# Performance work log

Hardware: AMD Instinct MI355X
Metric: run time of the kernel (lower is better)

The kernel has to match this reference:

```python
import jax, jax.numpy as jnp
import numpy as np
import math

B, T, D, H, K = 4, 2048, 1024, 16, 64

def setup_inputs() -> dict:
    key = jax.random.key(0)
    ks = jax.random.split(key, 6)
    scale = 1.0 / math.sqrt(D)  # keep logits in a sane range (torch code uses raw randn params)
    X = jax.random.normal(ks[0], (B, T, D), dtype=jnp.float32)
    Wq = jax.random.normal(ks[1], (H, D, K), dtype=jnp.float32) * scale
    Wk = jax.random.normal(ks[2], (H, D, K), dtype=jnp.float32) * scale
    Wv = jax.random.normal(ks[3], (H, D, K), dtype=jnp.float32) * scale
    Wo = jax.random.normal(ks[4], (H * K, H * K), dtype=jnp.float32) * (1.0 / math.sqrt(H * K))
    bo = jnp.zeros((H * K,), dtype=jnp.float32)
    return {"X": X, "Wq": Wq, "Wk": Wk, "Wv": Wv, "Wo": Wo, "bo": bo}

def reference(X, Wq, Wk, Wv, Wo, bo):
    # per-head projections: [B,H,T,K]
    q = jnp.einsum('btc,nck->bntk', X, Wq)
    k = jnp.einsum('btc,nck->bntk', X, Wk)
    v = jnp.einsum('btc,nck->bntk', X, Wv)
    # full score matrix [B,H,T,T] with causal mask (query t attends to s <= t)
    scores = jnp.einsum('bntk,bnsk->bnts', q, k) / math.sqrt(K)
    causal = jnp.tril(jnp.ones((T, T), dtype=bool))
    scores = jnp.where(causal[None, None], scores, jnp.finfo(scores.dtype).min)
    attn = jax.nn.softmax(scores, axis=-1)
    out = jnp.einsum('bnts,bnsk->bntk', attn, v)  # [B,H,T,K]
    # concat heads along feature dim (head-major ordering, matches torch.cat over heads)
    out = jnp.transpose(out, (0, 2, 1, 3)).reshape(B, T, H * K)
    # output projection (torch nn.Linear: x @ W.T + b)
    return out @ Wo.T + bo
```

## Files before the change

### kernel.cpp

```cpp
#include <hip/hip_runtime.h>
#include <hip/hip_bf16.h>
#include <math.h>

#define B_SZ 4
#define T_SZ 2048
#define D_SZ 1024
#define H_SZ 16
#define K_SZ 64

typedef __attribute__((ext_vector_type(8))) short bf8_t;
typedef __attribute__((ext_vector_type(4))) float f4_t;

__device__ __forceinline__ ushort f2bf(float f) {
    union { float f; unsigned u; } v; v.f = f;
    return (ushort)((v.u + 0x7fffu + ((v.u >> 16) & 1u)) >> 16);
}

__device__ __forceinline__ uint cvt_pk_bf16(float lo, float hi) {
    uint r;
    asm("v_cvt_pk_bf16_f32 %0, %1, %2" : "=v"(r) : "v"(lo), "v"(hi));
    return r;
}

__device__ __forceinline__ void gld_lds16(const ushort* g, ushort* l) {
    __builtin_amdgcn_global_load_lds(
        (const __attribute__((address_space(1))) void*)g,
        (__attribute__((address_space(3))) void*)l, 16, 0, 0);
}

#define Q_PRESCALE 0.18033688011112042f

__global__ __launch_bounds__(256) void convert_bf16_kernel(
    const float* __restrict__ src, ushort* __restrict__ dst)
{
    const size_t i = ((size_t)blockIdx.x * 256 + threadIdx.x) * 8;
    float4 a = *(const float4*)(src + i);
    float4 b = *(const float4*)(src + i + 4);
    ushort o[8] = {f2bf(a.x), f2bf(a.y), f2bf(a.z), f2bf(a.w),
                   f2bf(b.x), f2bf(b.y), f2bf(b.z), f2bf(b.w)};
    *(uint4*)(dst + i) = *(const uint4*)o;
}

__global__ __launch_bounds__(256) void transpose_w_kernel(
    const float* __restrict__ Wq, const float* __restrict__ Wk,
    const float* __restrict__ Wv, ushort* __restrict__ WT)
{
    __shared__ __align__(16) float tile[64][68];
    const int tid = threadIdx.x;
    const int d0  = blockIdx.x * 64;
    const int g   = blockIdx.y;
    const int sel = g >> 4, h = g & 15;
    const float* W = (sel == 0 ? Wq : (sel == 1 ? Wk : Wv)) + (size_t)h * D_SZ * K_SZ;

    {
        const int r = tid >> 2, ks = (tid & 3) * 16;
        const float4* src = (const float4*)(W + (size_t)(d0 + r) * 64 + ks);
        float4* dst = (float4*)&tile[r][ks];
        dst[0] = src[0]; dst[1] = src[1]; dst[2] = src[2]; dst[3] = src[3];
    }
    __syncthreads();
    {
        const int k = tid >> 2, ds = (tid & 3) * 16;
        ushort o[16];
        #pragma unroll
        for (int i = 0; i < 16; ++i) o[i] = f2bf(tile[ds + i][k]);
        uint4* dst = (uint4*)&WT[(size_t)(sel * 1024 + h * 64 + k) * 1024 + d0 + ds];
        dst[0] = ((const uint4*)o)[0];
        dst[1] = ((const uint4*)o)[1];
    }
}

__device__ __forceinline__ void gemm_bt_tile(
    const ushort* __restrict__ A, const ushort* __restrict__ Bt,
    int Kdim, int m0, int n0, ushort* As, ushort* Bs, f4_t acc[4][4])
{
    const int tid  = threadIdx.x;
    const int lane = tid & 63, wv = tid >> 6;
    const int l16  = lane & 15, quad = lane >> 4;
    const int wm   = (wv >> 1) * 64, wn = (wv & 1) * 64;
    const int sw   = (l16 >> 1) & 3;

    const int ra0 = tid >> 2,         qa0 = (tid & 3) ^ ((ra0 >> 1) & 3);
    const int ra1 = (tid + 256) >> 2, qa1 = (tid & 3) ^ ((ra1 >> 1) & 3);
    ushort* ldsA0 = As + (size_t)(wv * 64) * 8;
    ushort* ldsA1 = As + (size_t)(wv * 64 + 256) * 8;
    ushort* ldsB0 = Bs + (size_t)(wv * 64) * 8;
    ushort* ldsB1 = Bs + (size_t)(wv * 64 + 256) * 8;
    const ushort* gA0 = A  + (size_t)(m0 + ra0) * Kdim + qa0 * 8;
    const ushort* gA1 = A  + (size_t)(m0 + ra1) * Kdim + qa1 * 8;
    const ushort* gB0 = Bt + (size_t)(n0 + ra0) * Kdim + qa0 * 8;
    const ushort* gB1 = Bt + (size_t)(n0 + ra1) * Kdim + qa1 * 8;

    for (int k0 = 0; k0 < Kdim; k0 += 32) {
        __syncthreads();
        gld_lds16(gA0 + k0, ldsA0);
        gld_lds16(gA1 + k0, ldsA1);
        gld_lds16(gB0 + k0, ldsB0);
        gld_lds16(gB1 + k0, ldsB1);
        __syncthreads();

        bf8_t a[4], b[4];
        #pragma unroll
        for (int mt = 0; mt < 4; ++mt)
            a[mt] = *(const bf8_t*)&As[(wm + mt * 16 + l16) * 32 + ((quad ^ sw) * 8)];
        #pragma unroll
        for (int nt = 0; nt < 4; ++nt)
            b[nt] = *(const bf8_t*)&Bs[(wn + nt * 16 + l16) * 32 + ((quad ^ sw) * 8)];
        #pragma unroll
        for (int mt = 0; mt < 4; ++mt)
            #pragma unroll
            for (int nt = 0; nt < 4; ++nt)
                acc[mt][nt] = __builtin_amdgcn_mfma_f32_16x16x32_bf16(
                    a[mt], b[nt], acc[mt][nt], 0, 0, 0);
    }
}

__global__ __launch_bounds__(256) void gemm_qkv_kernel(
    const ushort* __restrict__ Xb, const ushort* __restrict__ WT,
    ushort* __restrict__ Qo, ushort* __restrict__ Ko, ushort* __restrict__ Vo)
{
    __shared__ __align__(16) ushort As[128 * 32];
    __shared__ __align__(16) ushort Bs[128 * 32];
    const int n0 = blockIdx.x * 128, m0 = blockIdx.y * 128;

    f4_t acc[4][4];
    #pragma unroll
    for (int i = 0; i < 4; ++i)
        #pragma unroll
        for (int j = 0; j < 4; ++j) acc[i][j] = (f4_t){0.f, 0.f, 0.f, 0.f};

    gemm_bt_tile(Xb, WT, 1024, m0, n0, As, Bs, acc);

    const int tid = threadIdx.x;
    const int lane = tid & 63, wv = tid >> 6;
    const int l16 = lane & 15, quad = lane >> 4;
    const int wm = (wv >> 1) * 64, wn = (wv & 1) * 64;
    const int sel = n0 >> 10;
    ushort* Out = (sel == 0 ? Qo : (sel == 1 ? Ko : Vo));
    const float osc = (sel == 0) ? Q_PRESCALE : 1.0f;

    #pragma unroll
    for (int nt = 0; nt < 4; ++nt) {
        const int col = n0 + wn + nt * 16 + l16;
        const int h = (col >> 6) & 15, kk = col & 63;
        #pragma unroll
        for (int mt = 0; mt < 4; ++mt) {
            #pragma unroll
            for (int r = 0; r < 4; ++r) {
                const int row = m0 + wm + mt * 16 + quad * 4 + r;
                const int bb = row >> 11, t = row & 2047;
                Out[((size_t)(bb * 16 + h) * 2048 + t) * 64 + kk] =
                    f2bf(acc[mt][nt][r] * osc);
            }
        }
    }
}

__global__ __launch_bounds__(256) void gemm_out_kernel(
    const ushort* __restrict__ Yb, const ushort* __restrict__ WoB,
    const float* __restrict__ bo, float* __restrict__ Out)
{
    __shared__ __align__(16) ushort As[128 * 32];
    __shared__ __align__(16) ushort Bs[128 * 32];
    const int n0 = blockIdx.x * 128, m0 = blockIdx.y * 128;

    f4_t acc[4][4];
    #pragma unroll
    for (int i = 0; i < 4; ++i)
        #pragma unroll
        for (int j = 0; j < 4; ++j) acc[i][j] = (f4_t){0.f, 0.f, 0.f, 0.f};

    gemm_bt_tile(Yb, WoB, 1024, m0, n0, As, Bs, acc);

    const int tid = threadIdx.x;
    const int lane = tid & 63, wv = tid >> 6;
    const int l16 = lane & 15, quad = lane >> 4;
    const int wm = (wv >> 1) * 64, wn = (wv & 1) * 64;

    #pragma unroll
    for (int nt = 0; nt < 4; ++nt) {
        const int col = n0 + wn + nt * 16 + l16;
        const float bias = bo[col];
        #pragma unroll
        for (int mt = 0; mt < 4; ++mt) {
            #pragma unroll
            for (int r = 0; r < 4; ++r) {
                const int row = m0 + wm + mt * 16 + quad * 4 + r;
                Out[(size_t)row * 1024 + col] = acc[mt][nt][r] + bias;
            }
        }
    }
}

__global__ __launch_bounds__(256) void transpose_v_kernel(
    const ushort* __restrict__ V, ushort* __restrict__ Vt)
{
    __shared__ __align__(16) ushort tile[64 * 74];
    const int tid = threadIdx.x;
    const int t0  = blockIdx.x * 64;
    const int bh  = blockIdx.y;

    {
        const int t = tid >> 2, ks = (tid & 3) * 16;
        const ushort* src = V + ((size_t)bh * T_SZ + t0 + t) * K_SZ + ks;
        uint4 a = *(const uint4*)src;
        uint4 b = *(const uint4*)(src + 8);
        uint* dst = (uint*)&tile[t * 74 + ks];
        dst[0] = a.x; dst[1] = a.y; dst[2] = a.z; dst[3] = a.w;
        dst[4] = b.x; dst[5] = b.y; dst[6] = b.z; dst[7] = b.w;
    }
    __syncthreads();
    {
        const int l = tid & 63, w = tid >> 6;
        #pragma unroll
        for (int kk = 0; kk < 16; ++kk) {
            const int k = w * 16 + kk;
            Vt[((size_t)bh * K_SZ + k) * T_SZ + t0 + l] = tile[l * 74 + k];
        }
    }
}

__global__ __launch_bounds__(64) void attn_mfma_kernel(
    const ushort* __restrict__ Qg, const ushort* __restrict__ Kg,
    const ushort* __restrict__ Vtg, ushort* __restrict__ Y)
{
    __shared__ __align__(16) ushort Ph[32 * 72];

    const int lane = threadIdx.x;
    const int l16  = lane & 15;
    const int quad = lane >> 4;

    const int lin  = blockIdx.x;
    const int xcd  = lin & 7;
    const int slot = (lin >> 3) & 31;
    const int u    = lin >> 8;
    const int bh   = xcd * 8 + (u & 7);
    const int j    = (u < 8) ? slot : 63 - slot;
    const int bb   = bh >> 4, h = bh & 15;

    const int trow = j * 32;

    const ushort* Kbh = Kg  + (size_t)bh * T_SZ * K_SZ;
    const ushort* Vbh = Vtg + (size_t)bh * K_SZ * T_SZ;

    bf8_t qa[2][2];
    #pragma unroll
    for (int mt = 0; mt < 2; ++mt) {
        const ushort* qp = Qg + ((size_t)bh * T_SZ + trow + mt * 16 + l16) * K_SZ + quad * 8;
        qa[mt][0] = *(const bf8_t*)qp;
        qa[mt][1] = *(const bf8_t*)(qp + 32);
    }

    f4_t O[2][4];
    float lp[2] = {0.f, 0.f};
    #pragma unroll
    for (int mt = 0; mt < 2; ++mt)
        #pragma unroll
        for (int dt = 0; dt < 4; ++dt) O[mt][dt] = (f4_t){0.f, 0.f, 0.f, 0.f};

    const int n_it = (trow + 32 + 63) >> 6;

    bf8_t kb[4][2], vb[4][2];
    #pragma unroll
    for (int nt = 0; nt < 4; ++nt)
        #pragma unroll
        for (int hh = 0; hh < 2; ++hh) {
            kb[nt][hh] = *(const bf8_t*)&Kbh[(size_t)(nt * 16 + l16) * K_SZ + hh * 32 + quad * 8];
            vb[nt][hh] = *(const bf8_t*)&Vbh[(size_t)(nt * 16 + l16) * T_SZ + hh * 32 + quad * 8];
        }

    for (int it = 0; it < n_it; ++it) {
        const int s0 = it * 64;
        const bool more = (it + 1 < n_it);
        const int  sn   = s0 + 64;

        f4_t S[4][2];
        #pragma unroll
        for (int nt = 0; nt < 4; ++nt)
            #pragma unroll
            for (int mt = 0; mt < 2; ++mt) {
                S[nt][mt] = (f4_t){0.f, 0.f, 0.f, 0.f};
                S[nt][mt] = __builtin_amdgcn_mfma_f32_16x16x32_bf16(
                    kb[nt][0], qa[mt][0], S[nt][mt], 0, 0, 0);
                S[nt][mt] = __builtin_amdgcn_mfma_f32_16x16x32_bf16(
                    kb[nt][1], qa[mt][1], S[nt][mt], 0, 0, 0);
            }

        if (more) {
            #pragma unroll
            for (int nt = 0; nt < 4; ++nt)
                #pragma unroll
                for (int hh = 0; hh < 2; ++hh)
                    kb[nt][hh] = *(const bf8_t*)&Kbh[
                        (size_t)(sn + nt * 16 + l16) * K_SZ + hh * 32 + quad * 8];
        }

        const bool diag = (s0 + 64 > trow);
        #pragma unroll
        for (int mt = 0; mt < 2; ++mt) {
            const int qg = trow + mt * 16 + l16;
            #pragma unroll
            for (int nt = 0; nt < 4; ++nt) {
                float p[4];
                if (diag) {
                    #pragma unroll
                    for (int r = 0; r < 4; ++r) {
                        float x = S[nt][mt][r];
                        if (s0 + nt * 16 + quad * 4 + r > qg) x = -1e30f;
                        p[r] = __builtin_amdgcn_exp2f(x);
                    }
                } else {
                    #pragma unroll
                    for (int r = 0; r < 4; ++r)
                        p[r] = __builtin_amdgcn_exp2f(S[nt][mt][r]);
                }
                lp[mt] += (p[0] + p[1]) + (p[2] + p[3]);
                uint2 pk;
                pk.x = cvt_pk_bf16(p[0], p[1]);
                pk.y = cvt_pk_bf16(p[2], p[3]);
                *(uint2*)&Ph[(mt * 16 + l16) * 72 + nt * 16 + quad * 4] = pk;
            }
        }
        asm volatile("" ::: "memory");
        bf8_t pa[2][2];
        #pragma unroll
        for (int mt = 0; mt < 2; ++mt) {
            const ushort* pr = &Ph[(mt * 16 + l16) * 72];
            pa[mt][0] = *(const bf8_t*)(pr + quad * 8);
            pa[mt][1] = *(const bf8_t*)(pr + 32 + quad * 8);
        }
        asm volatile("" ::: "memory");

        #pragma unroll
        for (int dt = 0; dt < 4; ++dt)
            #pragma unroll
            for (int mt = 0; mt < 2; ++mt) {
                O[mt][dt] = __builtin_amdgcn_mfma_f32_16x16x32_bf16(
                    pa[mt][0], vb[dt][0], O[mt][dt], 0, 0, 0);
                O[mt][dt] = __builtin_amdgcn_mfma_f32_16x16x32_bf16(
                    pa[mt][1], vb[dt][1], O[mt][dt], 0, 0, 0);
            }

        if (more) {
            #pragma unroll
            for (int nt = 0; nt < 4; ++nt)
                #pragma unroll
                for (int hh = 0; hh < 2; ++hh)
                    vb[nt][hh] = *(const bf8_t*)&Vbh[
                        (size_t)(nt * 16 + l16) * T_SZ + sn + hh * 32 + quad * 8];
        }
    }

    #pragma unroll
    for (int mt = 0; mt < 2; ++mt) {
        float s = lp[mt];
        s += __shfl_xor(s, 16);
        s += __shfl_xor(s, 32);
        const float inv = 1.f / s;
        float invr[4];
        #pragma unroll
        for (int r = 0; r < 4; ++r)
            invr[r] = __shfl(inv, quad * 4 + r);
        #pragma unroll
        for (int dt = 0; dt < 4; ++dt) {
            const int col = h * 64 + dt * 16 + l16;
            #pragma unroll
            for (int r = 0; r < 4; ++r) {
                const int tg = trow + mt * 16 + quad * 4 + r;
                Y[((size_t)(bb * T_SZ + tg)) * (H_SZ * K_SZ) + col] =
                    f2bf(O[mt][dt][r] * invr[r]);
            }
        }
    }
}

extern "C" void kernel_launch(void* const* d_in, const int* in_sizes, int n_in,
                              void* d_out, int out_size, void* d_ws, size_t ws_size,
                              hipStream_t stream) {
    const float* X  = (const float*)d_in[0];
    const float* Wq = (const float*)d_in[1];
    const float* Wk = (const float*)d_in[2];
    const float* Wv = (const float*)d_in[3];
    const float* Wo = (const float*)d_in[4];
    const float* bo = (const float*)d_in[5];
    float* out = (float*)d_out;

    const size_t NE = (size_t)B_SZ * H_SZ * T_SZ * K_SZ;
    ushort* Qb   = (ushort*)d_ws;
    ushort* Kb   = Qb + NE;
    ushort* Vb   = Kb + NE;
    ushort* Vtb  = Vb + NE;
    ushort* Yb   = Vtb + NE;
    ushort* Xb   = Yb + NE;
    ushort* WT   = Xb + NE;
    ushort* WoB  = WT + (size_t)3072 * 1024;

    convert_bf16_kernel<<<dim3(4096), 256, 0, stream>>>(X, Xb);
    convert_bf16_kernel<<<dim3(512), 256, 0, stream>>>(Wo, WoB);
    transpose_w_kernel<<<dim3(16, 48), 256, 0, stream>>>(Wq, Wk, Wv, WT);
    gemm_qkv_kernel<<<dim3(24, 64), 256, 0, stream>>>(Xb, WT, Qb, Kb, Vb);
    transpose_v_kernel<<<dim3(32, 64), 256, 0, stream>>>(Vb, Vtb);
    attn_mfma_kernel<<<dim3(4096), 64, 0, stream>>>(Qb, Kb, Vtb, Yb);
    gemm_out_kernel<<<dim3(8, 64), 256, 0, stream>>>(Yb, WoB, bo, out);
}
```

Baseline: 342.6 us.

## Balance causal attention work by pairing low and high query tiles per wave

Each wave now handles one 16-row query tile near the start and its mirrored tile near the end, so every wave runs a similar number of causal iterations. Each wave loads a K/V tile once and applies it to both query tiles, skipping the low tile once it is past its diagonal. Blocks hold two waves, and the grid changes from an XCD-swizzled 1D layout to a 2D (tile pair, batch-head) layout. This removes load imbalance between short and long causal rows, at the cost of the XCD-aware L2 locality mapping and possibly more K/V loads per query row.

```diff
diff --git a/kernel.cpp b/kernel.cpp
--- a/kernel.cpp
+++ b/kernel.cpp
@@ -220,45 +220,46 @@
     }
 }
 
-__global__ __launch_bounds__(64) void attn_mfma_kernel(
+__global__ __launch_bounds__(128) void attn_mfma_kernel(
     const ushort* __restrict__ Qg, const ushort* __restrict__ Kg,
     const ushort* __restrict__ Vtg, ushort* __restrict__ Y)
 {
-    __shared__ __align__(16) ushort Ph[32 * 72];
-
-    const int lane = threadIdx.x;
+    __shared__ __align__(16) ushort Ph[2][16 * 72];
+
+    const int tid  = threadIdx.x;
+    const int w    = tid >> 6;
+    const int lane = tid & 63;
     const int l16  = lane & 15;
     const int quad = lane >> 4;
 
-    const int lin  = blockIdx.x;
-    const int xcd  = lin & 7;
-    const int slot = (lin >> 3) & 31;
-    const int u    = lin >> 8;
-    const int bh   = xcd * 8 + (u & 7);
-    const int j    = (u < 8) ? slot : 63 - slot;
+    const int p    = (blockIdx.x << 1) | w;
+    const int bh   = blockIdx.y;
     const int bb   = bh >> 4, h = bh & 15;
 
-    const int trow = j * 32;
+    const int trowL = p * 16;
+    const int trowH = (127 - p) * 16;
 
     const ushort* Kbh = Kg  + (size_t)bh * T_SZ * K_SZ;
     const ushort* Vbh = Vtg + (size_t)bh * K_SZ * T_SZ;
 
-    bf8_t qa[2][2];
-    #pragma unroll
-    for (int mt = 0; mt < 2; ++mt) {
-        const ushort* qp = Qg + ((size_t)bh * T_SZ + trow + mt * 16 + l16) * K_SZ + quad * 8;
-        qa[mt][0] = *(const bf8_t*)qp;
-        qa[mt][1] = *(const bf8_t*)(qp + 32);
-    }
-
-    f4_t O[2][4];
-    float lp[2] = {0.f, 0.f};
-    #pragma unroll
-    for (int mt = 0; mt < 2; ++mt)
-        #pragma unroll
-        for (int dt = 0; dt < 4; ++dt) O[mt][dt] = (f4_t){0.f, 0.f, 0.f, 0.f};
-
-    const int n_it = (trow + 32 + 63) >> 6;
+    bf8_t qaL[2], qaH[2];
+    {
+        const ushort* qpL = Qg + ((size_t)bh * T_SZ + trowL + l16) * K_SZ + quad * 8;
+        const ushort* qpH = Qg + ((size_t)bh * T_SZ + trowH + l16) * K_SZ + quad * 8;
+        qaL[0] = *(const bf8_t*)qpL;  qaL[1] = *(const bf8_t*)(qpL + 32);
+        qaH[0] = *(const bf8_t*)qpH;  qaH[1] = *(const bf8_t*)(qpH + 32);
+    }
+
+    f4_t OL[4], OH[4];
+    float lpL = 0.f, lpH = 0.f;
+    #pragma unroll
+    for (int dt = 0; dt < 4; ++dt) {
+        OL[dt] = (f4_t){0.f, 0.f, 0.f, 0.f};
+        OH[dt] = (f4_t){0.f, 0.f, 0.f, 0.f};
+    }
+
+    ushort* myP = Ph[w];
+    const int n_it = (trowH + 16 + 63) >> 6;
 
     bf8_t kb[4][2], vb[4][2];
     #pragma unroll
@@ -269,22 +270,62 @@
             vb[nt][hh] = *(const bf8_t*)&Vbh[(size_t)(nt * 16 + l16) * T_SZ + hh * 32 + quad * 8];
         }
 
+    int s0 = 0;
+    auto qk = [&](const bf8_t (&qa)[2], f4_t (&S)[4]) {
+        #pragma unroll
+        for (int nt = 0; nt < 4; ++nt) {
+            S[nt] = (f4_t){0.f, 0.f, 0.f, 0.f};
+            S[nt] = __builtin_amdgcn_mfma_f32_16x16x32_bf16(kb[nt][0], qa[0], S[nt], 0, 0, 0);
+            S[nt] = __builtin_amdgcn_mfma_f32_16x16x32_bf16(kb[nt][1], qa[1], S[nt], 0, 0, 0);
+        }
+    };
+    auto sm_pv = [&](f4_t (&S)[4], f4_t (&O)[4], float& lp, int trow) {
+        const bool diag = (s0 + 64 > trow);
+        const int qg = trow + l16;
+        #pragma unroll
+        for (int nt = 0; nt < 4; ++nt) {
+            float pr[4];
+            if (diag) {
+                #pragma unroll
+                for (int r = 0; r < 4; ++r) {
+                    float x = S[nt][r];
+                    if (s0 + nt * 16 + quad * 4 + r > qg) x = -1e30f;
+                    pr[r] = __builtin_amdgcn_exp2f(x);
+                }
+            } else {
+                #pragma unroll
+                for (int r = 0; r < 4; ++r)
+                    pr[r] = __builtin_amdgcn_exp2f(S[nt][r]);
+            }
+            lp += (pr[0] + pr[1]) + (pr[2] + pr[3]);
+            uint2 pk;
+            pk.x = cvt_pk_bf16(pr[0], pr[1]);
+            pk.y = cvt_pk_bf16(pr[2], pr[3]);
+            *(uint2*)&myP[l16 * 72 + nt * 16 + quad * 4] = pk;
+        }
+        asm volatile("" ::: "memory");
+        bf8_t pa[2];
+        pa[0] = *(const bf8_t*)(&myP[l16 * 72] + quad * 8);
+        pa[1] = *(const bf8_t*)(&myP[l16 * 72] + 32 + quad * 8);
+        asm volatile("" ::: "memory");
+        #pragma unroll
+        for (int dt = 0; dt < 4; ++dt) {
+            O[dt] = __builtin_amdgcn_mfma_f32_16x16x32_bf16(pa[0], vb[dt][0], O[dt], 0, 0, 0);
+            O[dt] = __builtin_amdgcn_mfma_f32_16x16x32_bf16(pa[1], vb[dt][1], O[dt], 0, 0, 0);
+        }
+    };
+
     for (int it = 0; it < n_it; ++it) {
-        const int s0 = it * 64;
+        s0 = it * 64;
+        const bool doL  = (s0 < trowL + 16);
         const bool more = (it + 1 < n_it);
         const int  sn   = s0 + 64;
 
-        f4_t S[4][2];
-        #pragma unroll
-        for (int nt = 0; nt < 4; ++nt)
-            #pragma unroll
-            for (int mt = 0; mt < 2; ++mt) {
-                S[nt][mt] = (f4_t){0.f, 0.f, 0.f, 0.f};
-                S[nt][mt] = __builtin_amdgcn_mfma_f32_16x16x32_bf16(
-                    kb[nt][0], qa[mt][0], S[nt][mt], 0, 0, 0);
-                S[nt][mt] = __builtin_amdgcn_mfma_f32_16x16x32_bf16(
-                    kb[nt][1], qa[mt][1], S[nt][mt], 0, 0, 0);
-            }
+        f4_t S[4];
+        qk(qaH, S);
+        sm_pv(S, OH, lpH, trowH);
+
+        if (doL) qk(qaL, S);
 
         if (more) {
             #pragma unroll
@@ -295,51 +336,7 @@
                         (size_t)(sn + nt * 16 + l16) * K_SZ + hh * 32 + quad * 8];
         }
 
-        const bool diag = (s0 + 64 > trow);
-        #pragma unroll
-        for (int mt = 0; mt < 2; ++mt) {
-            const int qg = trow + mt * 16 + l16;
-            #pragma unroll
-            for (int nt = 0; nt < 4; ++nt) {
-                float p[4];
-                if (diag) {
-                    #pragma unroll
-                    for (int r = 0; r < 4; ++r) {
-                        float x = S[nt][mt][r];
-                        if (s0 + nt * 16 + quad * 4 + r > qg) x = -1e30f;
-                        p[r] = __builtin_amdgcn_exp2f(x);
-                    }
-                } else {
-                    #pragma unroll
-                    for (int r = 0; r < 4; ++r)
-                        p[r] = __builtin_amdgcn_exp2f(S[nt][mt][r]);
-                }
-                lp[mt] += (p[0] + p[1]) + (p[2] + p[3]);
-                uint2 pk;
-                pk.x = cvt_pk_bf16(p[0], p[1]);
-                pk.y = cvt_pk_bf16(p[2], p[3]);
-                *(uint2*)&Ph[(mt * 16 + l16) * 72 + nt * 16 + quad * 4] = pk;
-            }
-        }
-        asm volatile("" ::: "memory");
-        bf8_t pa[2][2];
-        #pragma unroll
-        for (int mt = 0; mt < 2; ++mt) {
-            const ushort* pr = &Ph[(mt * 16 + l16) * 72];
-            pa[mt][0] = *(const bf8_t*)(pr + quad * 8);
-            pa[mt][1] = *(const bf8_t*)(pr + 32 + quad * 8);
-        }
-        asm volatile("" ::: "memory");
-
-        #pragma unroll
-        for (int dt = 0; dt < 4; ++dt)
-            #pragma unroll
-            for (int mt = 0; mt < 2; ++mt) {
-                O[mt][dt] = __builtin_amdgcn_mfma_f32_16x16x32_bf16(
-                    pa[mt][0], vb[dt][0], O[mt][dt], 0, 0, 0);
-                O[mt][dt] = __builtin_amdgcn_mfma_f32_16x16x32_bf16(
-                    pa[mt][1], vb[dt][1], O[mt][dt], 0, 0, 0);
-            }
+        if (doL) sm_pv(S, OL, lpL, trowL);
 
         if (more) {
             #pragma unroll
@@ -351,9 +348,8 @@
         }
     }
 
-    #pragma unroll
-    for (int mt = 0; mt < 2; ++mt) {
-        float s = lp[mt];
+    auto epi = [&](f4_t (&O)[4], float lp, int trow) {
+        float s = lp;
         s += __shfl_xor(s, 16);
         s += __shfl_xor(s, 32);
         const float inv = 1.f / s;
@@ -366,12 +362,14 @@
             const int col = h * 64 + dt * 16 + l16;
             #pragma unroll
             for (int r = 0; r < 4; ++r) {
-                const int tg = trow + mt * 16 + quad * 4 + r;
+                const int tg = trow + quad * 4 + r;
                 Y[((size_t)(bb * T_SZ + tg)) * (H_SZ * K_SZ) + col] =
-                    f2bf(O[mt][dt][r] * invr[r]);
+                    f2bf(O[dt][r] * invr[r]);
             }
         }
-    }
+    };
+    epi(OH, lpH, trowH);
+    epi(OL, lpL, trowL);
 }
 
 extern "C" void kernel_launch(void* const* d_in, const int* in_sizes, int n_in,
@@ -400,6 +398,6 @@
     transpose_w_kernel<<<dim3(16, 48), 256, 0, stream>>>(Wq, Wk, Wv, WT);
     gemm_qkv_kernel<<<dim3(24, 64), 256, 0, stream>>>(Xb, WT, Qb, Kb, Vb);
     transpose_v_kernel<<<dim3(32, 64), 256, 0, stream>>>(Vb, Vtb);
-    attn_mfma_kernel<<<dim3(4096), 64, 0, stream>>>(Qb, Kb, Vtb, Yb);
+    attn_mfma_kernel<<<dim3(32, 64), 128, 0, stream>>>(Qb, Kb, Vtb, Yb);
     gemm_out_kernel<<<dim3(8, 64), 256, 0, stream>>>(Yb, WoB, bo, out);
 }
```

After: 421.0 us. 22.9% more time.
